# Performance work log

Hardware: AMD Instinct MI355X
Metric: run time of the kernel (lower is better)

Reference implementation:

```python
import jax, jax.numpy as jnp
import numpy as np

N_NODES = 100000
N_EDGES = 1600000
IN_FEATS = 256
HEADS = 4
OUT_FEATS = 32
NEG_SLOPE = 0.2


def setup_inputs() -> dict:
    key = jax.random.key(0)
    k = jax.random.split(key, 7)
    feat = jax.random.normal(k[0], (N_NODES, IN_FEATS), dtype=jnp.float32)
    src = jax.random.randint(k[1], (N_EDGES,), 0, N_NODES)
    dst = jax.random.randint(k[2], (N_EDGES,), 0, N_NODES)
    W = jax.random.normal(k[3], (HEADS * OUT_FEATS, IN_FEATS), dtype=jnp.float32) * 0.05
    attn_l = jax.random.normal(k[4], (1, HEADS, OUT_FEATS), dtype=jnp.float32) * 0.1
    attn_r = jax.random.normal(k[5], (1, HEADS, OUT_FEATS), dtype=jnp.float32) * 0.1
    bias = jnp.zeros((HEADS * OUT_FEATS,), dtype=jnp.float32)
    return {"feat": feat, "src": src, "dst": dst, "W": W,
            "attn_l": attn_l, "attn_r": attn_r, "bias": bias}


def reference(feat, src, dst, W, attn_l, attn_r, bias):
    N = feat.shape[0]
    H, F = attn_l.shape[1], attn_l.shape[2]
    # linear projection: [N, H*F] -> [N, H, F]
    ft = (feat @ W.T).reshape(N, H, F)
    # per-node attention scores [N, H]
    el = jnp.sum(ft * attn_l, axis=-1)
    er = jnp.sum(ft * attn_r, axis=-1)
    # edge scores: u_add_v + LeakyReLU, [E, H]
    e = el[src] + er[dst]
    e = jnp.where(e >= 0, e, NEG_SLOPE * e)
    # edge softmax segmented by destination node
    emax = jax.ops.segment_max(e, dst, num_segments=N)  # [N, H]
    emax = jnp.where(jnp.isfinite(emax), emax, 0.0)
    ex = jnp.exp(e - emax[dst])  # [E, H]
    esum = jax.ops.segment_sum(ex, dst, num_segments=N)  # [N, H]
    a = ex / jnp.maximum(esum[dst], 1e-16)  # [E, H]
    # weighted scatter-sum aggregation: u_mul_e + sum
    msg = ft[src] * a[:, :, None]  # [E, H, F]
    rst = jax.ops.segment_sum(msg, dst, num_segments=N)  # [N, H, F]
    rst = rst + bias.reshape(1, H, F)
    return rst


if __name__ == "__main__":
    out = reference(**setup_inputs())
    print(out.shape, out.dtype)
```

## Files before the change

### kernel.cpp

```cpp
#include <hip/hip_runtime.h>

#define NEG_SLOPE 0.2f
#define G_SHIFT 8
#define G_SIZE  256
#define NB1     256

typedef __attribute__((ext_vector_type(8))) short short8;
typedef __attribute__((ext_vector_type(4))) float floatx4;

__device__ inline unsigned short f32_to_bf16(float f) {
    union { float f; unsigned int u; } c; c.f = f;
    unsigned int u = c.u;
    u += 0x7FFFu + ((u >> 16) & 1u);
    return (unsigned short)(u >> 16);
}
__device__ inline float bf16_lo(unsigned int u) {
    union { unsigned int u; float f; } c; c.u = u << 16; return c.f;
}
__device__ inline float bf16_hi(unsigned int u) {
    union { unsigned int u; float f; } c; c.u = u & 0xFFFF0000u; return c.f;
}

__global__ __launch_bounds__(256) void k_wconv(const float* __restrict__ W,
                                               unsigned short* __restrict__ Wb,
                                               int n) {
    int i = blockIdx.x * 256 + threadIdx.x;
    if (i < n) Wb[i] = f32_to_bf16(W[i]);
}

__global__ __launch_bounds__(256) void k_gemm_mfma(const float* __restrict__ feat,
                                                   const unsigned short* __restrict__ Wb,
                                                   unsigned short* __restrict__ ftb,
                                                   int M) {
    __shared__ float Abuf[4][2048];

    const int tid  = threadIdx.x;
    const int w    = tid >> 6;
    const int lane = tid & 63;
    const int l16  = lane & 15;
    const int quad = lane >> 4;
    const int wm   = w & 1;
    const int wn   = w >> 1;
    const int tile = blockIdx.x * 64;

    short8 b[4][8];
#pragma unroll
    for (int t = 0; t < 4; ++t) {
        const unsigned short* bp =
            Wb + (size_t)((wn * 4 + t) * 16 + l16) * 256 + quad * 8;
#pragma unroll
        for (int kc = 0; kc < 8; ++kc)
            b[t][kc] = *(const short8*)(bp + kc * 32);
    }

    const int rloc = lane >> 3;
    const int c4   = ((lane & 7) ^ rloc) * 4;
    int gr0 = tile + (w * 2 + 0) * 8 + rloc; if (gr0 >= M) gr0 = M - 1;
    int gr1 = tile + (w * 2 + 1) * 8 + rloc; if (gr1 >= M) gr1 = M - 1;
    const float* g0 = feat + (size_t)gr0 * 256 + c4;
    const float* g1 = feat + (size_t)gr1 * 256 + c4;

#define STAGE(JC) do {                                                          \
    __builtin_amdgcn_global_load_lds(                                           \
        (const __attribute__((address_space(1))) unsigned int*)(g0 + (JC) * 32),\
        (__attribute__((address_space(3))) unsigned int*)&Abuf[(JC) & 3][(w * 2 + 0) * 256], \
        16, 0, 0);                                                              \
    __builtin_amdgcn_global_load_lds(                                           \
        (const __attribute__((address_space(1))) unsigned int*)(g1 + (JC) * 32),\
        (__attribute__((address_space(3))) unsigned int*)&Abuf[(JC) & 3][(w * 2 + 1) * 256], \
        16, 0, 0);                                                              \
} while (0)

    floatx4 acc[2][4];
#pragma unroll
    for (int m = 0; m < 2; ++m)
#pragma unroll
        for (int t = 0; t < 4; ++t)
            acc[m][t] = (floatx4){0.f, 0.f, 0.f, 0.f};

    STAGE(0); STAGE(1); STAGE(2);

    const int sw = (l16 & 7) << 4;

#define KSTEP(J, VM) do {                                                       \
    asm volatile("s_waitcnt vmcnt(" #VM ")" ::: "memory");                      \
    __builtin_amdgcn_s_barrier();                                               \
    asm volatile("" ::: "memory");                                              \
    if ((J) + 3 < 8) STAGE((J) + 3);                                            \
    const char* ab = (const char*)&Abuf[(J) & 3][0];                            \
    _Pragma("unroll")                                                           \
    for (int m = 0; m < 2; ++m) {                                               \
        int base = (wm * 32 + m * 16 + l16) * 128 + quad * 32;                  \
        float4 alo = *(const float4*)(ab + ((base)      ^ sw));                 \
        float4 ahi = *(const float4*)(ab + ((base + 16) ^ sw));                 \
        short8 af;                                                              \
        af[0] = (short)f32_to_bf16(alo.x);                                      \
        af[1] = (short)f32_to_bf16(alo.y);                                      \
        af[2] = (short)f32_to_bf16(alo.z);                                      \
        af[3] = (short)f32_to_bf16(alo.w);                                      \
        af[4] = (short)f32_to_bf16(ahi.x);                                      \
        af[5] = (short)f32_to_bf16(ahi.y);                                      \
        af[6] = (short)f32_to_bf16(ahi.z);                                      \
        af[7] = (short)f32_to_bf16(ahi.w);                                      \
        _Pragma("unroll")                                                       \
        for (int t = 0; t < 4; ++t)                                             \
            acc[m][t] = __builtin_amdgcn_mfma_f32_16x16x32_bf16(                \
                af, b[t][(J)], acc[m][t], 0, 0, 0);                             \
    }                                                                           \
} while (0)

    KSTEP(0, 4); KSTEP(1, 4); KSTEP(2, 4); KSTEP(3, 4);
    KSTEP(4, 4); KSTEP(5, 4); KSTEP(6, 2); KSTEP(7, 0);

#undef KSTEP
#undef STAGE

#pragma unroll
    for (int m = 0; m < 2; ++m) {
#pragma unroll
        for (int t = 0; t < 4; ++t) {
#pragma unroll
            for (int r = 0; r < 4; ++r) {
                int row = tile + wm * 32 + m * 16 + quad * 4 + r;
                if (row < M)
                    ftb[(size_t)row * 128 + (wn * 4 + t) * 16 + l16] =
                        f32_to_bf16(acc[m][t][r]);
            }
        }
    }
}

__global__ __launch_bounds__(256) void k_elr(const unsigned short* __restrict__ ftb,
                                             const float* __restrict__ al,
                                             const float* __restrict__ ar,
                                             float* __restrict__ el,
                                             float* __restrict__ er,
                                             int NH) {
    int i = blockIdx.x * 256 + threadIdx.x;
    if (i >= NH) return;
    int h = i & 3;
    const unsigned int* f = (const unsigned int*)ftb + (size_t)i * 16;
    const float* lp = al + h * 32;
    const float* rp = ar + h * 32;
    float sl = 0.f, sr = 0.f;
#pragma unroll
    for (int j = 0; j < 16; ++j) {
        unsigned int u = f[j];
        float f0 = bf16_lo(u), f1 = bf16_hi(u);
        sl += f0 * lp[2 * j] + f1 * lp[2 * j + 1];
        sr += f0 * rp[2 * j] + f1 * rp[2 * j + 1];
    }
    el[i] = sl;
    er[i] = sr;
}

__global__ __launch_bounds__(256) void k_count(const int* __restrict__ dst,
                                               int* __restrict__ counts,
                                               int E, int CH, int B) {
    __shared__ int hist[512];
    int j = blockIdx.x, t = threadIdx.x;
    for (int bk = t; bk < B; bk += 256) hist[bk] = 0;
    __syncthreads();
    int lo = j * CH, hi = min(E, lo + CH);
    for (int i = lo + t; i < hi; i += 256)
        atomicAdd(&hist[dst[i] >> G_SHIFT], 1);
    __syncthreads();
    for (int bk = t; bk < B; bk += 256) counts[bk * NB1 + j] = hist[bk];
}

__global__ __launch_bounds__(256) void k_scan1(const int* __restrict__ deg,
                                               int* __restrict__ offs,
                                               int* __restrict__ bsum, int n) {
    __shared__ int ls[256];
    int b = blockIdx.x, t = threadIdx.x;
    int base = b * 1024 + t * 4;
    int d0 = (base + 0 < n) ? deg[base + 0] : 0;
    int d1 = (base + 1 < n) ? deg[base + 1] : 0;
    int d2 = (base + 2 < n) ? deg[base + 2] : 0;
    int d3 = (base + 3 < n) ? deg[base + 3] : 0;
    int s = d0 + d1 + d2 + d3;
    ls[t] = s;
    __syncthreads();
    for (int o = 1; o < 256; o <<= 1) {
        int v = (t >= o) ? ls[t - o] : 0;
        __syncthreads();
        ls[t] += v;
        __syncthreads();
    }
    int excl = ls[t] - s;
    if (base + 0 < n) offs[base + 0] = excl;
    if (base + 1 < n) offs[base + 1] = excl + d0;
    if (base + 2 < n) offs[base + 2] = excl + d0 + d1;
    if (base + 3 < n) offs[base + 3] = excl + d0 + d1 + d2;
    if (t == 255) bsum[b] = ls[255];
}

__global__ __launch_bounds__(256) void k_scan2(int* __restrict__ bsum, int NB) {
    __shared__ int ls[256];
    int t = threadIdx.x;
    int v = (t < NB) ? bsum[t] : 0;
    ls[t] = v;
    __syncthreads();
    for (int o = 1; o < 256; o <<= 1) {
        int u = (t >= o) ? ls[t - o] : 0;
        __syncthreads();
        ls[t] += u;
        __syncthreads();
    }
    if (t < NB) bsum[t] = ls[t] - v;
}

__global__ __launch_bounds__(256) void k_partition(const int* __restrict__ src,
                                                   const int* __restrict__ dst,
                                                   const int* __restrict__ scanned,
                                                   const int* __restrict__ bsum,
                                                   int* __restrict__ part,
                                                   int E, int CH, int B) {
    __shared__ int curs[512];
    int j = blockIdx.x, t = threadIdx.x;
    for (int bk = t; bk < B; bk += 256) {
        int idx = bk * NB1 + j;
        curs[bk] = scanned[idx] + bsum[idx >> 10];
    }
    __syncthreads();
    int lo = j * CH, hi = min(E, lo + CH);
    for (int i = lo + t; i < hi; i += 256) {
        int d = dst[i];
        int bk = d >> G_SHIFT;
        int pos = atomicAdd(&curs[bk], 1);
        if (pos >= 0 && pos < E)
            part[pos] = ((d & (G_SIZE - 1)) << 17) | src[i];
    }
}

__global__ __launch_bounds__(256) void k_bucket(const int* __restrict__ scanned,
                                                const int* __restrict__ bsum,
                                                const int* __restrict__ part,
                                                int* __restrict__ offs,
                                                int* __restrict__ esrc,
                                                int E, int B, int N) {
    __shared__ int hist[256], ls[256], curs[256];
    int b = blockIdx.x, t = threadIdx.x;
    int i0 = b * NB1;
    int start = scanned[i0] + bsum[i0 >> 10];
    int end = E;
    if (b < B - 1) {
        int i1 = (b + 1) * NB1;
        end = scanned[i1] + bsum[i1 >> 10];
    }

    hist[t] = 0;
    __syncthreads();
    for (int i = start + t; i < end; i += 256)
        atomicAdd(&hist[(part[i] >> 17) & 255], 1);
    __syncthreads();

    int h = hist[t];
    ls[t] = h;
    __syncthreads();
    for (int o = 1; o < 256; o <<= 1) {
        int v = (t >= o) ? ls[t - o] : 0;
        __syncthreads();
        ls[t] += v;
        __syncthreads();
    }
    int excl = ls[t] - h;
    curs[t] = excl;
    int node = b * G_SIZE + t;
    if (node < N) offs[node] = start + excl;
    if (b == B - 1 && t == 0) offs[N] = E;
    __syncthreads();

    for (int i = start + t; i < end; i += 256) {
        int p = part[i];
        int pos = start + atomicAdd(&curs[(p >> 17) & 255], 1);
        if (pos >= 0 && pos < E) esrc[pos] = p & 0x1FFFF;
    }
}

__global__ __launch_bounds__(256) void k_aggr_csr(const int* __restrict__ offs,
                                                  const int* __restrict__ esrc,
                                                  const float* __restrict__ el,
                                                  const float* __restrict__ er,
                                                  const unsigned short* __restrict__ ftb,
                                                  const float* __restrict__ bias,
                                                  float* __restrict__ out,
                                                  int N) {
    int node = blockIdx.x * 4 + (threadIdx.x >> 6);
    if (node >= N) return;
    int lane = threadIdx.x & 63;
    int h1 = lane & 3;
    int h2b = (lane >> 4) << 2;
    float er1 = er[node * 4 + h1];

    int start = offs[node];
    int deg   = offs[node + 1] - start;

    float2 acc = make_float2(0.f, 0.f);
    float  wsum = 0.f;
    const unsigned int* ftu = (const unsigned int*)ftb;

    int p = 0;
    while (p < deg) {
        int cnt = min(16, deg - p);
        float w = 0.f;
        int   s = 0;
        int   e = lane >> 2;
        if (e < cnt) {
            s = esrc[start + p + e];
            float x = el[s * 4 + h1] + er1;
            x = x >= 0.f ? x : NEG_SLOPE * x;
            w = __expf(x);
        }
        float        wv[16];
        unsigned int uv[16];
#pragma unroll
        for (int j = 0; j < 16; ++j) {
            int ib = (j << 4) + h2b;
            wv[j] = __int_as_float(
                __builtin_amdgcn_ds_bpermute(ib, __float_as_int(w)));
            int sj = __builtin_amdgcn_ds_bpermute(ib, s);
            uv[j] = ftu[(size_t)sj * 64 + lane];
        }
#pragma unroll
        for (int j = 0; j < 16; ++j) {
            wsum  += wv[j];
            acc.x += wv[j] * bf16_lo(uv[j]);
            acc.y += wv[j] * bf16_hi(uv[j]);
        }
        p += cnt;
    }
    float scale = 1.0f / fmaxf(wsum, 1e-16f);
    float2 bv = ((const float2*)bias)[lane];
    float2 o;
    o.x = acc.x * scale + bv.x;
    o.y = acc.y * scale + bv.y;
    ((float2*)out)[(size_t)node * 64 + lane] = o;
}

__global__ __launch_bounds__(256) void k_init_fb(float* __restrict__ out,
                                                 const float* __restrict__ bias,
                                                 float* __restrict__ esum,
                                                 int n_out, int n_esum) {
    int i = blockIdx.x * 256 + threadIdx.x;
    if (i < n_out)  out[i]  = bias[i & 127];
    if (i < n_esum) esum[i] = 0.0f;
}

__global__ __launch_bounds__(256) void k_esum_fb(const int* __restrict__ src,
                                                 const int* __restrict__ dst,
                                                 const float* __restrict__ el,
                                                 const float* __restrict__ er,
                                                 float* __restrict__ esum,
                                                 int E4) {
    int i = blockIdx.x * 256 + threadIdx.x;
    if (i >= E4) return;
    int e = i >> 2, h = i & 3;
    int s = src[e], d = dst[e];
    float x = el[s * 4 + h] + er[d * 4 + h];
    x = x >= 0.f ? x : NEG_SLOPE * x;
    atomicAdd(&esum[d * 4 + h], __expf(x));
}

__global__ __launch_bounds__(256) void k_aggr_fb(const int* __restrict__ src,
                                                 const int* __restrict__ dst,
                                                 const float* __restrict__ el,
                                                 const float* __restrict__ er,
                                                 const float* __restrict__ esum,
                                                 const unsigned short* __restrict__ ftb,
                                                 float* __restrict__ out,
                                                 int E) {
    int i = blockIdx.x * 256 + threadIdx.x;
    int e = i >> 6;
    if (e >= E) return;
    int c = i & 63;
    int h = c >> 4;
    int s = src[e], d = dst[e];
    float x = el[s * 4 + h] + er[d * 4 + h];
    x = x >= 0.f ? x : NEG_SLOPE * x;
    float a = __expf(x) / fmaxf(esum[d * 4 + h], 1e-16f);
    unsigned int u = ((const unsigned int*)ftb)[(size_t)s * 64 + c];
    float* o = out + (size_t)d * 128 + c * 2;
    atomicAdd(o + 0, bf16_lo(u) * a);
    atomicAdd(o + 1, bf16_hi(u) * a);
}

extern "C" void kernel_launch(void* const* d_in, const int* in_sizes, int n_in,
                              void* d_out, int out_size, void* d_ws, size_t ws_size,
                              hipStream_t stream) {
    const float* feat   = (const float*)d_in[0];
    const int*   src    = (const int*)d_in[1];
    const int*   dst    = (const int*)d_in[2];
    const float* W      = (const float*)d_in[3];
    const float* attn_l = (const float*)d_in[4];
    const float* attn_r = (const float*)d_in[5];
    const float* bias   = (const float*)d_in[6];

    const int N  = in_sizes[0] / 256;
    const int E  = in_sizes[1];
    const int NW = in_sizes[3];
    float* out = (float*)d_out;

    const int B  = (N + G_SIZE - 1) / G_SIZE;
    const int CH = (E + NB1 - 1) / NB1;
    const int n2 = B * NB1;

    unsigned short* ftb = (unsigned short*)d_ws;
    unsigned short* Wb  = ftb + (size_t)N * 128;
    float* el = (float*)(Wb + NW);
    float* er = el + (size_t)N * 4;
    int* offs    = (int*)(er + (size_t)N * 4);
    int* counts  = offs + (N + 1);
    int* scanned = counts + n2;
    int* bsum    = scanned + n2;
    int* part    = bsum + 256;
    int* esrc    = part + E;
    size_t need = (size_t)((char*)(esrc + E) - (char*)d_ws);

    k_wconv<<<(NW + 255) / 256, 256, 0, stream>>>(W, Wb, NW);
    k_gemm_mfma<<<(N + 63) / 64, 256, 0, stream>>>(feat, Wb, ftb, N);
    k_elr<<<(N * 4 + 255) / 256, 256, 0, stream>>>(ftb, attn_l, attn_r, el, er, N * 4);

    if (ws_size >= need) {
        const int NBs = (n2 + 1023) / 1024;
        k_count<<<NB1, 256, 0, stream>>>(dst, counts, E, CH, B);
        k_scan1<<<NBs, 256, 0, stream>>>(counts, scanned, bsum, n2);
        k_scan2<<<1, 256, 0, stream>>>(bsum, NBs);
        k_partition<<<NB1, 256, 0, stream>>>(src, dst, scanned, bsum, part, E, CH, B);
        k_bucket<<<B, 256, 0, stream>>>(scanned, bsum, part, offs, esrc, E, B, N);
        k_aggr_csr<<<(N + 3) / 4, 256, 0, stream>>>(offs, esrc, el, er, ftb, bias, out, N);
    } else {
        float* esum = (float*)(er + (size_t)N * 4);
        k_init_fb<<<(N * 128 + 255) / 256, 256, 0, stream>>>(out, bias, esum, N * 128, N * 4);
        k_esum_fb<<<(E * 4 + 255) / 256, 256, 0, stream>>>(src, dst, el, er, esum, E * 4);
        k_aggr_fb<<<((size_t)E * 64 + 255) / 256, 256, 0, stream>>>(src, dst, el, er, esum, ftb, out, E);
    }
}
```

Before: 343.2 us.

## Precompute edge attention weights during bucketing and stream them in aggregation

The bucketing kernel now computes exp(LeakyReLU(el[src]+er[dst])) per edge, with er staged in shared memory, and writes a float4 per edge alongside the sorted source index. The aggregation kernel reads these contiguous weights instead of gathering el and recomputing scores, and stages weights and indices through shared memory. This removes per-edge score computation and random el reads from the aggregation pass. In exchange it adds a per-edge weight buffer write and read, and keeps the old kernel as a fallback when workspace is insufficient.

```diff
diff --git a/kernel.cpp b/kernel.cpp
--- a/kernel.cpp
+++ b/kernel.cpp
@@ -236,10 +236,14 @@
 __global__ __launch_bounds__(256) void k_bucket(const int* __restrict__ scanned,
                                                 const int* __restrict__ bsum,
                                                 const int* __restrict__ part,
+                                                const float* __restrict__ el,
+                                                const float* __restrict__ er,
                                                 int* __restrict__ offs,
                                                 int* __restrict__ esrc,
-                                                int E, int B, int N) {
+                                                float4* __restrict__ wbuf,
+                                                int do_w, int E, int B, int N) {
     __shared__ int hist[256], ls[256], curs[256];
+    __shared__ float4 er_s[256];
     int b = blockIdx.x, t = threadIdx.x;
     int i0 = b * NB1;
     int start = scanned[i0] + bsum[i0 >> 10];
@@ -250,6 +254,9 @@
     }
 
     hist[t] = 0;
+    int nd = b * G_SIZE + t;
+    er_s[t] = (do_w && nd < N) ? ((const float4*)er)[nd]
+                               : make_float4(0.f, 0.f, 0.f, 0.f);
     __syncthreads();
     for (int i = start + t; i < end; i += 256)
         atomicAdd(&hist[(part[i] >> 17) & 255], 1);
@@ -266,26 +273,98 @@
     }
     int excl = ls[t] - h;
     curs[t] = excl;
-    int node = b * G_SIZE + t;
-    if (node < N) offs[node] = start + excl;
+    if (nd < N) offs[nd] = start + excl;
     if (b == B - 1 && t == 0) offs[N] = E;
     __syncthreads();
 
     for (int i = start + t; i < end; i += 256) {
         int p = part[i];
-        int pos = start + atomicAdd(&curs[(p >> 17) & 255], 1);
-        if (pos >= 0 && pos < E) esrc[pos] = p & 0x1FFFF;
+        int ld = (p >> 17) & 255;
+        int s  = p & 0x1FFFF;
+        int pos = start + atomicAdd(&curs[ld], 1);
+        if (pos >= 0 && pos < E) {
+            esrc[pos] = s;
+            if (do_w) {
+                float4 elv = *(const float4*)(el + (size_t)s * 4);
+                float4 erv = er_s[ld];
+                float4 w4;
+                float x;
+                x = elv.x + erv.x; x = x >= 0.f ? x : NEG_SLOPE * x; w4.x = __expf(x);
+                x = elv.y + erv.y; x = x >= 0.f ? x : NEG_SLOPE * x; w4.y = __expf(x);
+                x = elv.z + erv.z; x = x >= 0.f ? x : NEG_SLOPE * x; w4.z = __expf(x);
+                x = elv.w + erv.w; x = x >= 0.f ? x : NEG_SLOPE * x; w4.w = __expf(x);
+                wbuf[pos] = w4;
+            }
+        }
     }
 }
 
 __global__ __launch_bounds__(256) void k_aggr_csr(const int* __restrict__ offs,
                                                   const int* __restrict__ esrc,
-                                                  const float* __restrict__ el,
-                                                  const float* __restrict__ er,
+                                                  const float* __restrict__ wbuf,
                                                   const unsigned short* __restrict__ ftb,
                                                   const float* __restrict__ bias,
                                                   float* __restrict__ out,
                                                   int N) {
+    __shared__ float smw[4][64];
+    __shared__ int   sms[4][64];
+    int wv = threadIdx.x >> 6;
+    int node = blockIdx.x * 4 + wv;
+    if (node >= N) return;
+    int lane = threadIdx.x & 63;
+    int h2 = lane >> 4;
+
+    int start = offs[node];
+    int deg   = offs[node + 1] - start;
+
+    float2 acc = make_float2(0.f, 0.f);
+    float  wsum = 0.f;
+    const unsigned int* ftu = (const unsigned int*)ftb;
+
+    int p = 0;
+    while (p < deg) {
+        int cnt = min(16, deg - p);
+        int e = lane >> 2;
+        float wl = 0.f;
+        int   sl = 0;
+        if (e < cnt) {
+            wl = wbuf[(size_t)(start + p) * 4 + lane];
+            sl = esrc[start + p + e];
+        }
+        smw[wv][lane] = wl;
+        sms[wv][lane] = sl;
+        float        wv16[16];
+        unsigned int uv[16];
+#pragma unroll
+        for (int j = 0; j < 16; ++j) {
+            wv16[j] = smw[wv][4 * j + h2];
+            int sj  = sms[wv][4 * j + h2];
+            uv[j] = ftu[(size_t)sj * 64 + lane];
+        }
+#pragma unroll
+        for (int j = 0; j < 16; ++j) {
+            wsum  += wv16[j];
+            acc.x += wv16[j] * bf16_lo(uv[j]);
+            acc.y += wv16[j] * bf16_hi(uv[j]);
+        }
+        p += cnt;
+    }
+    float scale = 1.0f / fmaxf(wsum, 1e-16f);
+    float2 bv = ((const float2*)bias)[lane];
+    float2 o;
+    o.x = acc.x * scale + bv.x;
+    o.y = acc.y * scale + bv.y;
+    ((float2*)out)[(size_t)node * 64 + lane] = o;
+}
+
+__global__ __launch_bounds__(256) void k_aggr_csr_old(const int* __restrict__ offs,
+                                                      const int* __restrict__ esrc,
+                                                      const float* __restrict__ el,
+                                                      const float* __restrict__ er,
+                                                      const unsigned short* __restrict__ ftb,
+                                                      const float* __restrict__ bias,
+                                                      float* __restrict__ out,
+                                                      int N) {
     int node = blockIdx.x * 4 + (threadIdx.x >> 6);
     if (node >= N) return;
     int lane = threadIdx.x & 63;
@@ -415,20 +494,29 @@
     int* bsum    = scanned + n2;
     int* part    = bsum + 256;
     int* esrc    = part + E;
-    size_t need = (size_t)((char*)(esrc + E) - (char*)d_ws);
+    float4* wbuf = (float4*)(((uintptr_t)(esrc + E) + 15) & ~(uintptr_t)15);
+    size_t need_w   = (size_t)((char*)(wbuf + E) - (char*)d_ws);
+    size_t need_old = (size_t)((char*)(esrc + E) - (char*)d_ws);
 
     k_wconv<<<(NW + 255) / 256, 256, 0, stream>>>(W, Wb, NW);
     k_gemm_mfma<<<(N + 63) / 64, 256, 0, stream>>>(feat, Wb, ftb, N);
     k_elr<<<(N * 4 + 255) / 256, 256, 0, stream>>>(ftb, attn_l, attn_r, el, er, N * 4);
 
-    if (ws_size >= need) {
+    if (ws_size >= need_old) {
+        const int do_w = (ws_size >= need_w) ? 1 : 0;
         const int NBs = (n2 + 1023) / 1024;
         k_count<<<NB1, 256, 0, stream>>>(dst, counts, E, CH, B);
         k_scan1<<<NBs, 256, 0, stream>>>(counts, scanned, bsum, n2);
         k_scan2<<<1, 256, 0, stream>>>(bsum, NBs);
         k_partition<<<NB1, 256, 0, stream>>>(src, dst, scanned, bsum, part, E, CH, B);
-        k_bucket<<<B, 256, 0, stream>>>(scanned, bsum, part, offs, esrc, E, B, N);
-        k_aggr_csr<<<(N + 3) / 4, 256, 0, stream>>>(offs, esrc, el, er, ftb, bias, out, N);
+        k_bucket<<<B, 256, 0, stream>>>(scanned, bsum, part, el, er, offs, esrc,
+                                        wbuf, do_w, E, B, N);
+        if (do_w)
+            k_aggr_csr<<<(N + 3) / 4, 256, 0, stream>>>(offs, esrc, (const float*)wbuf,
+                                                        ftb, bias, out, N);
+        else
+            k_aggr_csr_old<<<(N + 3) / 4, 256, 0, stream>>>(offs, esrc, el, er,
+                                                            ftb, bias, out, N);
     } else {
         float* esum = (float*)(er + (size_t)N * 4);
         k_init_fb<<<(N * 128 + 255) / 256, 256, 0, stream>>>(out, bias, esum, N * 128, N * 4);
```

Result: slower. 360.3 us (+5.0%).

## Replace two-level bucket CSR build with per-node atomic scatter and precomputed edge weights

Applied to the files above, without the earlier changes.

Replaces the bucketed two-pass partition (count, partition, bucket) with a per-node degree histogram built by global atomics, a scan, and a single atomic scatter into CSR order. The scatter also computes the LeakyReLU and exp edge weights for all four heads and stores them as float4 next to the source index. The aggregation kernel then reads precomputed weights and broadcasts them through shared memory instead of gathering el per edge and using ds_bpermute. This trades locality-friendly bucketing for many random global atomics and scattered writes, and adds a 16-byte-per-edge weight buffer.

```diff
diff --git a/kernel.cpp b/kernel.cpp
--- a/kernel.cpp
+++ b/kernel.cpp
@@ -1,9 +1,6 @@
 #include <hip/hip_runtime.h>
 
 #define NEG_SLOPE 0.2f
-#define G_SHIFT 8
-#define G_SIZE  256
-#define NB1     256
 
 typedef __attribute__((ext_vector_type(8))) short short8;
 typedef __attribute__((ext_vector_type(4))) float floatx4;
@@ -26,6 +23,11 @@
                                                int n) {
     int i = blockIdx.x * 256 + threadIdx.x;
     if (i < n) Wb[i] = f32_to_bf16(W[i]);
+}
+
+__global__ __launch_bounds__(256) void k_zero(int* __restrict__ p, int n) {
+    int i = blockIdx.x * 256 + threadIdx.x;
+    if (i < n) p[i] = 0;
 }
 
 __global__ __launch_bounds__(256) void k_gemm_mfma(const float* __restrict__ feat,
@@ -154,18 +156,10 @@
     er[i] = sr;
 }
 
-__global__ __launch_bounds__(256) void k_count(const int* __restrict__ dst,
-                                               int* __restrict__ counts,
-                                               int E, int CH, int B) {
-    __shared__ int hist[512];
-    int j = blockIdx.x, t = threadIdx.x;
-    for (int bk = t; bk < B; bk += 256) hist[bk] = 0;
-    __syncthreads();
-    int lo = j * CH, hi = min(E, lo + CH);
-    for (int i = lo + t; i < hi; i += 256)
-        atomicAdd(&hist[dst[i] >> G_SHIFT], 1);
-    __syncthreads();
-    for (int bk = t; bk < B; bk += 256) counts[bk * NB1 + j] = hist[bk];
+__global__ __launch_bounds__(256) void k_deg(const int* __restrict__ dst,
+                                             int* __restrict__ deg, int E) {
+    int i = blockIdx.x * 256 + threadIdx.x;
+    if (i < E) atomicAdd(&deg[dst[i]], 1);
 }
 
 __global__ __launch_bounds__(256) void k_scan1(const int* __restrict__ deg,
@@ -210,88 +204,60 @@
     if (t < NB) bsum[t] = ls[t] - v;
 }
 
-__global__ __launch_bounds__(256) void k_partition(const int* __restrict__ src,
-                                                   const int* __restrict__ dst,
-                                                   const int* __restrict__ scanned,
-                                                   const int* __restrict__ bsum,
-                                                   int* __restrict__ part,
-                                                   int E, int CH, int B) {
-    __shared__ int curs[512];
-    int j = blockIdx.x, t = threadIdx.x;
-    for (int bk = t; bk < B; bk += 256) {
-        int idx = bk * NB1 + j;
-        curs[bk] = scanned[idx] + bsum[idx >> 10];
-    }
-    __syncthreads();
-    int lo = j * CH, hi = min(E, lo + CH);
-    for (int i = lo + t; i < hi; i += 256) {
-        int d = dst[i];
-        int bk = d >> G_SHIFT;
-        int pos = atomicAdd(&curs[bk], 1);
-        if (pos >= 0 && pos < E)
-            part[pos] = ((d & (G_SIZE - 1)) << 17) | src[i];
-    }
-}
-
-__global__ __launch_bounds__(256) void k_bucket(const int* __restrict__ scanned,
-                                                const int* __restrict__ bsum,
-                                                const int* __restrict__ part,
-                                                int* __restrict__ offs,
-                                                int* __restrict__ esrc,
-                                                int E, int B, int N) {
-    __shared__ int hist[256], ls[256], curs[256];
-    int b = blockIdx.x, t = threadIdx.x;
-    int i0 = b * NB1;
-    int start = scanned[i0] + bsum[i0 >> 10];
-    int end = E;
-    if (b < B - 1) {
-        int i1 = (b + 1) * NB1;
-        end = scanned[i1] + bsum[i1 >> 10];
-    }
-
-    hist[t] = 0;
-    __syncthreads();
-    for (int i = start + t; i < end; i += 256)
-        atomicAdd(&hist[(part[i] >> 17) & 255], 1);
-    __syncthreads();
-
-    int h = hist[t];
-    ls[t] = h;
-    __syncthreads();
-    for (int o = 1; o < 256; o <<= 1) {
-        int v = (t >= o) ? ls[t - o] : 0;
-        __syncthreads();
-        ls[t] += v;
-        __syncthreads();
-    }
-    int excl = ls[t] - h;
-    curs[t] = excl;
-    int node = b * G_SIZE + t;
-    if (node < N) offs[node] = start + excl;
-    if (b == B - 1 && t == 0) offs[N] = E;
-    __syncthreads();
-
-    for (int i = start + t; i < end; i += 256) {
-        int p = part[i];
-        int pos = start + atomicAdd(&curs[(p >> 17) & 255], 1);
-        if (pos >= 0 && pos < E) esrc[pos] = p & 0x1FFFF;
+__global__ __launch_bounds__(256) void k_cursinit(const int* __restrict__ scanned,
+                                                  const int* __restrict__ bsum,
+                                                  int* __restrict__ offs,
+                                                  int* __restrict__ curs,
+                                                  int N, int E) {
+    int i = blockIdx.x * 256 + threadIdx.x;
+    if (i < N) {
+        int v = scanned[i] + bsum[i >> 10];
+        offs[i] = v;
+        curs[i] = v;
+    }
+    if (i == 0) offs[N] = E;
+}
+
+__global__ __launch_bounds__(256) void k_scatter(const int* __restrict__ src,
+                                                 const int* __restrict__ dst,
+                                                 const float* __restrict__ el,
+                                                 const float* __restrict__ er,
+                                                 int* __restrict__ curs,
+                                                 int* __restrict__ esrc,
+                                                 float4* __restrict__ wbuf,
+                                                 int E) {
+    int i = blockIdx.x * 256 + threadIdx.x;
+    if (i >= E) return;
+    int s = src[i], d = dst[i];
+    float4 elv = ((const float4*)el)[s];
+    float4 erv = ((const float4*)er)[d];
+    float4 w4;
+    float x;
+    x = elv.x + erv.x; x = x >= 0.f ? x : NEG_SLOPE * x; w4.x = __expf(x);
+    x = elv.y + erv.y; x = x >= 0.f ? x : NEG_SLOPE * x; w4.y = __expf(x);
+    x = elv.z + erv.z; x = x >= 0.f ? x : NEG_SLOPE * x; w4.z = __expf(x);
+    x = elv.w + erv.w; x = x >= 0.f ? x : NEG_SLOPE * x; w4.w = __expf(x);
+    int pos = atomicAdd(&curs[d], 1);
+    if (pos >= 0 && pos < E) {
+        esrc[pos] = s;
+        wbuf[pos] = w4;
     }
 }
 
 __global__ __launch_bounds__(256) void k_aggr_csr(const int* __restrict__ offs,
                                                   const int* __restrict__ esrc,
-                                                  const float* __restrict__ el,
-                                                  const float* __restrict__ er,
+                                                  const float* __restrict__ wbuf,
                                                   const unsigned short* __restrict__ ftb,
                                                   const float* __restrict__ bias,
                                                   float* __restrict__ out,
                                                   int N) {
-    int node = blockIdx.x * 4 + (threadIdx.x >> 6);
+    __shared__ float smw[4][64];
+    __shared__ int   sms[4][64];
+    int wv = threadIdx.x >> 6;
+    int node = blockIdx.x * 4 + wv;
     if (node >= N) return;
     int lane = threadIdx.x & 63;
-    int h1 = lane & 3;
-    int h2b = (lane >> 4) << 2;
-    float er1 = er[node * 4 + h1];
+    int h2 = lane >> 4;
 
     int start = offs[node];
     int deg   = offs[node + 1] - start;
@@ -303,30 +269,28 @@
     int p = 0;
     while (p < deg) {
         int cnt = min(16, deg - p);
-        float w = 0.f;
-        int   s = 0;
-        int   e = lane >> 2;
+        int e = lane >> 2;
+        float wl = 0.f;
+        int   sl = 0;
         if (e < cnt) {
-            s = esrc[start + p + e];
-            float x = el[s * 4 + h1] + er1;
-            x = x >= 0.f ? x : NEG_SLOPE * x;
-            w = __expf(x);
+            wl = wbuf[(size_t)(start + p) * 4 + lane];
+            sl = esrc[start + p + e];
         }
-        float        wv[16];
+        smw[wv][lane] = wl;
+        sms[wv][lane] = sl;
+        float        wv16[16];
         unsigned int uv[16];
 #pragma unroll
         for (int j = 0; j < 16; ++j) {
-            int ib = (j << 4) + h2b;
-            wv[j] = __int_as_float(
-                __builtin_amdgcn_ds_bpermute(ib, __float_as_int(w)));
-            int sj = __builtin_amdgcn_ds_bpermute(ib, s);
+            wv16[j] = smw[wv][4 * j + h2];
+            int sj  = sms[wv][4 * j + h2];
             uv[j] = ftu[(size_t)sj * 64 + lane];
         }
 #pragma unroll
         for (int j = 0; j < 16; ++j) {
-            wsum  += wv[j];
-            acc.x += wv[j] * bf16_lo(uv[j]);
-            acc.y += wv[j] * bf16_hi(uv[j]);
+            wsum  += wv16[j];
+            acc.x += wv16[j] * bf16_lo(uv[j]);
+            acc.y += wv16[j] * bf16_hi(uv[j]);
         }
         p += cnt;
     }
@@ -401,34 +365,34 @@
     const int NW = in_sizes[3];
     float* out = (float*)d_out;
 
-    const int B  = (N + G_SIZE - 1) / G_SIZE;
-    const int CH = (E + NB1 - 1) / NB1;
-    const int n2 = B * NB1;
-
     unsigned short* ftb = (unsigned short*)d_ws;
     unsigned short* Wb  = ftb + (size_t)N * 128;
     float* el = (float*)(Wb + NW);
     float* er = el + (size_t)N * 4;
     int* offs    = (int*)(er + (size_t)N * 4);
-    int* counts  = offs + (N + 1);
-    int* scanned = counts + n2;
-    int* bsum    = scanned + n2;
-    int* part    = bsum + 256;
-    int* esrc    = part + E;
-    size_t need = (size_t)((char*)(esrc + E) - (char*)d_ws);
+    int* deg     = offs + (N + 1);
+    int* scanned = deg + N;
+    int* bsum    = scanned + N;
+    int* curs    = bsum + 256;
+    int* esrc    = curs + N;
+    float4* wbuf = (float4*)(((uintptr_t)(esrc + E) + 15) & ~(uintptr_t)15);
+    size_t need = (size_t)((char*)(wbuf + E) - (char*)d_ws);
 
     k_wconv<<<(NW + 255) / 256, 256, 0, stream>>>(W, Wb, NW);
     k_gemm_mfma<<<(N + 63) / 64, 256, 0, stream>>>(feat, Wb, ftb, N);
     k_elr<<<(N * 4 + 255) / 256, 256, 0, stream>>>(ftb, attn_l, attn_r, el, er, N * 4);
 
     if (ws_size >= need) {
-        const int NBs = (n2 + 1023) / 1024;
-        k_count<<<NB1, 256, 0, stream>>>(dst, counts, E, CH, B);
-        k_scan1<<<NBs, 256, 0, stream>>>(counts, scanned, bsum, n2);
+        const int NBs = (N + 1023) / 1024;
+        k_zero<<<(N + 255) / 256, 256, 0, stream>>>(deg, N);
+        k_deg<<<(E + 255) / 256, 256, 0, stream>>>(dst, deg, E);
+        k_scan1<<<NBs, 256, 0, stream>>>(deg, scanned, bsum, N);
         k_scan2<<<1, 256, 0, stream>>>(bsum, NBs);
-        k_partition<<<NB1, 256, 0, stream>>>(src, dst, scanned, bsum, part, E, CH, B);
-        k_bucket<<<B, 256, 0, stream>>>(scanned, bsum, part, offs, esrc, E, B, N);
-        k_aggr_csr<<<(N + 3) / 4, 256, 0, stream>>>(offs, esrc, el, er, ftb, bias, out, N);
+        k_cursinit<<<(N + 255) / 256, 256, 0, stream>>>(scanned, bsum, offs, curs, N, E);
+        k_scatter<<<(E + 255) / 256, 256, 0, stream>>>(src, dst, el, er, curs,
+                                                       esrc, wbuf, E);
+        k_aggr_csr<<<(N + 3) / 4, 256, 0, stream>>>(offs, esrc, (const float*)wbuf,
+                                                    ftb, bias, out, N);
     } else {
         float* esum = (float*)(er + (size_t)N * 4);
         k_init_fb<<<(N * 128 + 255) / 256, 256, 0, stream>>>(out, bias, esum, N * 128, N * 4);
```

New measurement: 459.2 us. +33.8%, slower.
